# Kernel tuning notes

Measured on AMD Instinct MI355X. Metric: run time of the kernel, lower is better.

Reference implementation:

```python
import jax, jax.numpy as jnp
import numpy as np
import math

B, S, H = 2, 4096, 768
NH, HD = 12, 64  # num heads, head dim


def setup_inputs() -> dict:
    key = jax.random.key(0)
    ks = jax.random.split(key, 4)
    scale = 1.0 / math.sqrt(H)
    return {
        "hidden_states": jax.random.normal(ks[0], (B, S, H), jnp.float32),
        "attention_mask": jnp.zeros((B, 1, 1, S), jnp.float32),
        "Wq": jax.random.normal(ks[1], (H, H), jnp.float32) * scale,
        "bq": jnp.zeros((H,), jnp.float32),
        "Wk": jax.random.normal(ks[2], (H, H), jnp.float32) * scale,
        "bk": jnp.zeros((H,), jnp.float32),
        "Wv": jax.random.normal(ks[3], (H, H), jnp.float32) * scale,
        "bv": jnp.zeros((H,), jnp.float32),
    }


def reference(hidden_states, attention_mask, Wq, bq, Wk, bk, Wv, bv):
    # Linear projections (torch nn.Linear: x @ W.T + b)
    q = hidden_states @ Wq.T + bq  # [B,S,H]
    k = hidden_states @ Wk.T + bk
    v = hidden_states @ Wv.T + bv
    # split heads -> [B, NH, S, HD]
    def split(x):
        return x.reshape(B, S, NH, HD).transpose(0, 2, 1, 3)
    qh, kh, vh = split(q), split(k), split(v)
    scores = jnp.einsum('bhqd,bhkd->bhqk', qh, kh) / math.sqrt(HD)
    scores = scores + attention_mask  # additive mask, broadcast
    probs = jax.nn.softmax(scores, axis=-1)
    # dropout prob = 0.0 (inference) -> identity
    ctx = jnp.einsum('bhqk,bhkd->bhqd', probs, vh)
    ctx = ctx.transpose(0, 2, 1, 3).reshape(B, S, H)
    return ctx
```

## Files before the change

kernel.cpp:

```cpp
#include <hip/hip_runtime.h>
#include <hip/hip_bf16.h>

typedef float f32x4 __attribute__((ext_vector_type(4)));
typedef float f32x16 __attribute__((ext_vector_type(16)));
typedef short short8 __attribute__((ext_vector_type(8)));

#define LOG2E 1.44269504088896340736f

__device__ __forceinline__ ushort f2bf(float f){
  unsigned u = __builtin_bit_cast(unsigned, f);
  u = (u + 0x7fffu + ((u >> 16) & 1u)) >> 16;
  return (ushort)u;
}

__device__ __forceinline__ float exp2_hw(float x){
  float r; asm("v_exp_f32 %0, %1" : "=v"(r) : "v"(x)); return r;
}

__device__ __forceinline__ double pk_add(double a, double b){
  double d; asm("v_pk_add_f32 %0, %1, %2" : "=v"(d) : "v"(a), "v"(b)); return d;
}
__device__ __forceinline__ double pk_mul(double a, double b){
  double d; asm("v_pk_mul_f32 %0, %1, %2" : "=v"(d) : "v"(a), "v"(b)); return d;
}
__device__ __forceinline__ uint cvtpk_bf16(float lo, float hi){
  uint r; asm("v_cvt_pk_bf16_f32 %0, %1, %2" : "=v"(r) : "v"(lo), "v"(hi)); return r;
}
__device__ __forceinline__ double f2d(float x, float y){
  union { float f[2]; double d; } u; u.f[0] = x; u.f[1] = y; return u.d;
}
__device__ __forceinline__ float fmax3(float a, float b, float c){
  return fmaxf(fmaxf(a, b), c);
}

union F16u { f32x16 v; double d[8]; float f[16]; };

__global__ void prep_kernel(const float* __restrict__ hidden,
                            const float* __restrict__ Wq,
                            const float* __restrict__ Wk,
                            const float* __restrict__ Wv,
                            const float* __restrict__ mask,
                            ushort* __restrict__ Xb,
                            ushort* __restrict__ Wqb,
                            ushort* __restrict__ Wkb,
                            ushort* __restrict__ Wvb,
                            float* __restrict__ maskL){
  const int bid = blockIdx.x;
  if (bid < 6144 + 3*576){
    const float* src; ushort* dst; int i;
    if (bid < 6144){
      src = hidden; dst = Xb;  i = bid*256 + threadIdx.x;
    } else if (bid < 6144 + 576){
      src = Wq; dst = Wqb;     i = (bid - 6144)*256 + threadIdx.x;
    } else if (bid < 6144 + 1152){
      src = Wk; dst = Wkb;     i = (bid - 6720)*256 + threadIdx.x;
    } else {
      src = Wv; dst = Wvb;     i = (bid - 7296)*256 + threadIdx.x;
    }
    float4 v = ((const float4*)src)[i];
    ushort4 o; o.x = f2bf(v.x); o.y = f2bf(v.y); o.z = f2bf(v.z); o.w = f2bf(v.w);
    ((ushort4*)dst)[i] = o;
  } else {
    int i = (bid - 7872)*256 + threadIdx.x;
    float4 v = ((const float4*)mask)[i];
    float4 o;
    o.x = v.x * LOG2E; o.y = v.y * LOG2E; o.z = v.z * LOG2E; o.w = v.w * LOG2E;
    ((float4*)maskL)[i] = o;
  }
}

__global__ __launch_bounds__(256) void qkv_fused(const ushort* __restrict__ Xb,
                                                 const ushort* __restrict__ Wqb,
                                                 const ushort* __restrict__ Wkb,
                                                 const ushort* __restrict__ Wvb,
                                                 const float* __restrict__ bqp,
                                                 const float* __restrict__ bkp,
                                                 const float* __restrict__ bvp,
                                                 ushort* __restrict__ Qo,
                                                 ushort* __restrict__ Ko,
                                                 ushort* __restrict__ Vto,
                                                 float qscale){
  __shared__ ushort Xs[128*64];
  __shared__ ushort Ws[128*64];
  const int sel = blockIdx.y / 6;
  const int m0 = blockIdx.x * 128, n0 = (blockIdx.y % 6) * 128;
  const ushort* Wb  = (sel == 0) ? Wqb : (sel == 1) ? Wkb : Wvb;
  const float* bias = (sel == 0) ? bqp : (sel == 1) ? bkp : bvp;
  const int tid = threadIdx.x, w = tid >> 6, lane = tid & 63;
  const int r = lane & 15, g = lane >> 4;
  const int wr = (w >> 1) * 64, wc = (w & 1) * 64;
  const int lrow = lane >> 3;
  const int gk = (lane & 7) ^ lrow;
  f32x4 acc[4][4] = {};
  for (int k0 = 0; k0 < 768; k0 += 64){
    #pragma unroll
    for (int p = 0; p < 4; p++){
      int rowb = p*32 + w*8;
      int row = rowb + lrow;
      __builtin_amdgcn_global_load_lds(
        (const uint4*)(Xb + (size_t)(m0+row)*768 + k0 + gk*8),
        (uint4*)((char*)Xs + rowb*128), 16, 0, 0);
      __builtin_amdgcn_global_load_lds(
        (const uint4*)(Wb + (size_t)(n0+row)*768 + k0 + gk*8),
        (uint4*)((char*)Ws + rowb*128), 16, 0, 0);
    }
    __syncthreads();
    #pragma unroll
    for (int ks = 0; ks < 2; ks++){
      short8 af[4], bf[4];
      int bo = ks*64 + g*16;
      #pragma unroll
      for (int i = 0; i < 4; i++){
        int rowa = wr + i*16 + r;
        af[i] = *(const short8*)((char*)Xs + rowa*128 + (bo ^ ((rowa&7)<<4)));
        int rowb2 = wc + i*16 + r;
        bf[i] = *(const short8*)((char*)Ws + rowb2*128 + (bo ^ ((rowb2&7)<<4)));
      }
      #pragma unroll
      for (int i = 0; i < 4; i++)
        #pragma unroll
        for (int j = 0; j < 4; j++)
          acc[i][j] = __builtin_amdgcn_mfma_f32_16x16x32_bf16(af[i], bf[j], acc[i][j], 0,0,0);
    }
    __syncthreads();
  }
  if (sel < 2){
    ushort* Out = sel ? Ko : Qo;
    float scale = sel ? 1.0f : qscale;
    #pragma unroll
    for (int i = 0; i < 4; i++){
      #pragma unroll
      for (int j = 0; j < 4; j++){
        int col = n0 + wc + j*16 + r;
        float bv = bias[col];
        int rowb = m0 + wr + i*16 + g*4;
        #pragma unroll
        for (int q = 0; q < 4; q++)
          Out[(size_t)(rowb+q)*768 + col] = f2bf((acc[i][j][q] + bv) * scale);
      }
    }
  } else {
    #pragma unroll
    for (int i = 0; i < 4; i++){
      #pragma unroll
      for (int j = 0; j < 4; j++){
        int col = n0 + wc + j*16 + r;
        float bv = bias[col];
        int rowb = m0 + wr + i*16 + g*4;
        ushort4 o;
        o.x = f2bf(acc[i][j][0] + bv);
        o.y = f2bf(acc[i][j][1] + bv);
        o.z = f2bf(acc[i][j][2] + bv);
        o.w = f2bf(acc[i][j][3] + bv);
        size_t vrow = (size_t)((rowb >> 12) * 768 + col);
        *(ushort4*)(Vto + vrow * 4096 + (rowb & 4095)) = o;
      }
    }
  }
}

__global__ __launch_bounds__(256, 3) void flash_attn(const ushort* __restrict__ Qb,
                                                     const ushort* __restrict__ Kb,
                                                     const ushort* __restrict__ Vt,
                                                     const float* __restrict__ maskL,
                                                     ushort* __restrict__ part0,
                                                     ushort* __restrict__ part1,
                                                     float2* __restrict__ lm){
  __shared__ ushort SMEM[16384];
  const int tid = threadIdx.x, w = tid >> 6, lane = tid & 63;
  const int q = lane & 31, hi = lane >> 5;
  const int swq = (q & 7) << 4;
  const int h = blockIdx.y, b = blockIdx.z;
  const int qt = blockIdx.x >> 1, half = blockIdx.x & 1;
  const int q0 = qt * 128 + w * 32;
  char* sm = (char*)SMEM;

  short8 bq[4];
  {
    const ushort* qp = Qb + (size_t)(b*4096 + q0 + q)*768 + h*64 + hi*8;
    #pragma unroll
    for (int kd = 0; kd < 4; kd++) bq[kd] = *(const short8*)(qp + 16*kd);
  }
  const ushort* Kbase = Kb + (size_t)(b*4096 + half*2048)*768 + h*64;
  const ushort* Vbase = Vt + (size_t)(b*768 + h*64)*4096 + half*2048;

  const int row0 = tid >> 3, cir = tid & 7;
  const int row1 = row0 + 32;
  const int wb0 = row0*128 + ((cir*16) ^ ((row0&7)<<4));
  const int wb1 = row1*128 + ((cir*16) ^ ((row1&7)<<4));
  const ushort* kp0 = Kbase + (size_t)row0*768 + cir*8;
  const ushort* kp1 = Kbase + (size_t)row1*768 + cir*8;
  const ushort* vp0 = Vbase + (size_t)row0*4096 + cir*8;
  const ushort* vp1 = Vbase + (size_t)row1*4096 + cir*8;

  int off4[4];
  #pragma unroll
  for (int kd = 0; kd < 4; kd++)
    off4[kd] = q*128 + ((32*kd + 16*hi) ^ swq);

  uint4 k0r = *(const uint4*)kp0, k1r = *(const uint4*)kp1;
  uint4 v0r = *(const uint4*)vp0, v1r = *(const uint4*)vp1;
  *(uint4*)(sm + wb0) = k0r;           *(uint4*)(sm + wb1) = k1r;
  *(uint4*)(sm + 16384 + wb0) = v0r;   *(uint4*)(sm + 16384 + wb1) = v1r;
  k0r = *(const uint4*)(kp0 + (size_t)64*768);
  k1r = *(const uint4*)(kp1 + (size_t)64*768);
  v0r = *(const uint4*)(vp0 + 64);
  v1r = *(const uint4*)(vp1 + 64);
  __syncthreads();

  F16u c0, c1;
  { f32x16 zz = {}; c0.v = zz; c1.v = zz; }
  float mrun = -1e30f, lrun = 0.f;

  for (int t = 0; t < 32; t++){
    const int tb = (t & 1) << 13;
    const char* kb = sm + tb;
    const char* vb = kb + 16384;
    __builtin_amdgcn_s_setprio(1);
    f32x16 z0 = {}, z1 = {};
    #pragma unroll
    for (int kd = 0; kd < 4; kd++){
      short8 ak = *(const short8*)(kb + off4[kd]);
      z0 = __builtin_amdgcn_mfma_f32_32x32x16_bf16(ak, bq[kd], z0, 0,0,0);
    }
    #pragma unroll
    for (int kd = 0; kd < 4; kd++){
      short8 ak = *(const short8*)(kb + 4096 + off4[kd]);
      z1 = __builtin_amdgcn_mfma_f32_32x32x16_bf16(ak, bq[kd], z1, 0,0,0);
    }
    __builtin_amdgcn_s_setprio(0);
    F16u s0, s1; s0.v = z0; s1.v = z1;
    if (t < 31){
      char* wbuf = sm + (tb ^ 8192);
      *(uint4*)(wbuf + wb0) = k0r;           *(uint4*)(wbuf + wb1) = k1r;
      *(uint4*)(wbuf + 16384 + wb0) = v0r;   *(uint4*)(wbuf + 16384 + wb1) = v1r;
    }
    if (t < 30){
      const size_t kn = (size_t)(t+2) * 64;
      k0r = *(const uint4*)(kp0 + kn*768);
      k1r = *(const uint4*)(kp1 + kn*768);
      v0r = *(const uint4*)(vp0 + kn);
      v1r = *(const uint4*)(vp1 + kn);
    }
    const float* mrow = maskL + b*4096 + half*2048 + t*64 + hi*4;
    #pragma unroll
    for (int eq = 0; eq < 4; eq++){
      float4 m0v = *(const float4*)(mrow + eq*8);
      s0.d[2*eq]   = pk_add(s0.d[2*eq],   f2d(m0v.x, m0v.y));
      s0.d[2*eq+1] = pk_add(s0.d[2*eq+1], f2d(m0v.z, m0v.w));
      float4 m1v = *(const float4*)(mrow + 32 + eq*8);
      s1.d[2*eq]   = pk_add(s1.d[2*eq],   f2d(m1v.x, m1v.y));
      s1.d[2*eq+1] = pk_add(s1.d[2*eq+1], f2d(m1v.z, m1v.w));
    }
    float ma = fmax3(s0.f[0], s0.f[1], s0.f[2]);
    float mb = fmax3(s0.f[3], s0.f[4], s0.f[5]);
    ma = fmax3(ma, s0.f[6], s0.f[7]);
    mb = fmax3(mb, s0.f[8], s0.f[9]);
    ma = fmax3(ma, s0.f[10], s0.f[11]);
    mb = fmax3(mb, s0.f[12], s0.f[13]);
    ma = fmax3(ma, s0.f[14], s0.f[15]);
    mb = fmax3(mb, s1.f[0], s1.f[1]);
    ma = fmax3(ma, s1.f[2], s1.f[3]);
    mb = fmax3(mb, s1.f[4], s1.f[5]);
    ma = fmax3(ma, s1.f[6], s1.f[7]);
    mb = fmax3(mb, s1.f[8], s1.f[9]);
    ma = fmax3(ma, s1.f[10], s1.f[11]);
    mb = fmax3(mb, s1.f[12], s1.f[13]);
    float mt = fmax3(ma, s1.f[14], fmaxf(mb, s1.f[15]));
    mt = fmaxf(mt, __shfl_xor(mt, 32, 64));
    if (!__all(mt <= mrun + 11.5415603f)){
      float mnew = fmaxf(mrun, mt);
      float alpha = exp2_hw(mrun - mnew);
      mrun = mnew;
      lrun *= alpha;
      double al2 = f2d(alpha, alpha);
      #pragma unroll
      for (int i = 0; i < 8; i++){
        c0.d[i] = pk_mul(c0.d[i], al2);
        c1.d[i] = pk_mul(c1.d[i], al2);
      }
    }
    double msub = f2d(-mrun, -mrun);
    #pragma unroll
    for (int i = 0; i < 8; i++){
      s0.d[i] = pk_add(s0.d[i], msub);
      s1.d[i] = pk_add(s1.d[i], msub);
    }
    #pragma unroll
    for (int e = 0; e < 16; e++){
      s0.f[e] = exp2_hw(s0.f[e]);
      s1.f[e] = exp2_hw(s1.f[e]);
    }
    double t00 = pk_add(s0.d[0], s0.d[1]), t01 = pk_add(s0.d[2], s0.d[3]);
    double t02 = pk_add(s0.d[4], s0.d[5]), t03 = pk_add(s0.d[6], s0.d[7]);
    double t10 = pk_add(s1.d[0], s1.d[1]), t11 = pk_add(s1.d[2], s1.d[3]);
    double t12 = pk_add(s1.d[4], s1.d[5]), t13 = pk_add(s1.d[6], s1.d[7]);
    double u0 = pk_add(t00, t01), u1 = pk_add(t02, t03);
    double u2 = pk_add(t10, t11), u3 = pk_add(t12, t13);
    double wsum = pk_add(pk_add(u0, u1), pk_add(u2, u3));
    {
      union { double d; float f[2]; } uw; uw.d = wsum;
      float rs = uw.f[0] + uw.f[1];
      rs += __shfl_xor(rs, 32, 64);
      lrun += rs;
    }
    short8 bp[4];
    {
      uint pw[8];
      #pragma unroll
      for (int u = 0; u < 8; u++) pw[u] = cvtpk_bf16(s0.f[2*u], s0.f[2*u+1]);
      #pragma unroll
      for (int u2 = 0; u2 < 2; u2++){
        uint x0 = pw[4*u2+0], x1 = pw[4*u2+1], x2 = pw[4*u2+2], x3 = pw[4*u2+3];
        asm("v_permlane32_swap_b32 %0, %1" : "+v"(x0), "+v"(x2));
        asm("v_permlane32_swap_b32 %0, %1" : "+v"(x1), "+v"(x3));
        union { uint u[4]; short8 v; } bb;
        bb.u[0] = x0; bb.u[1] = x1; bb.u[2] = x2; bb.u[3] = x3;
        bp[u2] = bb.v;
      }
      #pragma unroll
      for (int u = 0; u < 8; u++) pw[u] = cvtpk_bf16(s1.f[2*u], s1.f[2*u+1]);
      #pragma unroll
      for (int u2 = 0; u2 < 2; u2++){
        uint x0 = pw[4*u2+0], x1 = pw[4*u2+1], x2 = pw[4*u2+2], x3 = pw[4*u2+3];
        asm("v_permlane32_swap_b32 %0, %1" : "+v"(x0), "+v"(x2));
        asm("v_permlane32_swap_b32 %0, %1" : "+v"(x1), "+v"(x3));
        union { uint u[4]; short8 v; } bb;
        bb.u[0] = x0; bb.u[1] = x1; bb.u[2] = x2; bb.u[3] = x3;
        bp[2+u2] = bb.v;
      }
    }
    __builtin_amdgcn_s_setprio(1);
    #pragma unroll
    for (int kk = 0; kk < 4; kk++){
      short8 av = *(const short8*)(vb + off4[kk]);
      c0.v = __builtin_amdgcn_mfma_f32_32x32x16_bf16(av, bp[kk], c0.v, 0,0,0);
    }
    #pragma unroll
    for (int kk = 0; kk < 4; kk++){
      short8 av = *(const short8*)(vb + 4096 + off4[kk]);
      c1.v = __builtin_amdgcn_mfma_f32_32x32x16_bf16(av, bp[kk], c1.v, 0,0,0);
    }
    __builtin_amdgcn_s_setprio(0);
    __syncthreads();
  }
  ushort* part = half ? part1 : part0;
  size_t orow = (size_t)(b*4096 + q0 + q) * 768 + h*64;
  #pragma unroll
  for (int eq = 0; eq < 4; eq++){
    uint2 o;
    o.x = cvtpk_bf16(c0.f[4*eq+0], c0.f[4*eq+1]);
    o.y = cvtpk_bf16(c0.f[4*eq+2], c0.f[4*eq+3]);
    *(uint2*)(part + orow + eq*8 + hi*4) = o;
  }
  #pragma unroll
  for (int eq = 0; eq < 4; eq++){
    uint2 o;
    o.x = cvtpk_bf16(c1.f[4*eq+0], c1.f[4*eq+1]);
    o.y = cvtpk_bf16(c1.f[4*eq+2], c1.f[4*eq+3]);
    *(uint2*)(part + orow + 32 + eq*8 + hi*4) = o;
  }
  if (hi == 0){
    int idx = ((half*2 + b)*12 + h)*4096 + (q0 + q);
    lm[idx] = make_float2(mrun, lrun);
  }
}

__global__ void merge_kernel(const ushort* __restrict__ p0, const ushort* __restrict__ p1,
                             const float2* __restrict__ lm, float* __restrict__ out){
  int i = blockIdx.x * 256 + threadIdx.x;
  const int nf4 = 2*4096*768/4;
  if (i >= nf4) return;
  int f = i * 4;
  int b = f / (4096*768);
  int rem = f - b*(4096*768);
  int qrow = rem / 768;
  int col = rem - qrow*768;
  int head = col >> 6;
  float2 L0 = lm[((    b)*12 + head)*4096 + qrow];
  float2 L1 = lm[((2 + b)*12 + head)*4096 + qrow];
  float M = fmaxf(L0.x, L1.x);
  float e0 = exp2f(L0.x - M), e1 = exp2f(L1.x - M);
  float inv = 1.0f / (L0.y*e0 + L1.y*e1);
  float s0 = e0 * inv, s1 = e1 * inv;
  uint2 a = ((const uint2*)p0)[i];
  uint2 c = ((const uint2*)p1)[i];
  float4 o;
  o.x = __builtin_bit_cast(float, a.x << 16)         * s0 + __builtin_bit_cast(float, c.x << 16)         * s1;
  o.y = __builtin_bit_cast(float, a.x & 0xffff0000u) * s0 + __builtin_bit_cast(float, c.x & 0xffff0000u) * s1;
  o.z = __builtin_bit_cast(float, a.y << 16)         * s0 + __builtin_bit_cast(float, c.y << 16)         * s1;
  o.w = __builtin_bit_cast(float, a.y & 0xffff0000u) * s0 + __builtin_bit_cast(float, c.y & 0xffff0000u) * s1;
  ((float4*)out)[i] = o;
}

extern "C" void kernel_launch(void* const* d_in, const int* in_sizes, int n_in,
                              void* d_out, int out_size, void* d_ws, size_t ws_size,
                              hipStream_t stream){
  const float* hidden = (const float*)d_in[0];
  const float* mask   = (const float*)d_in[1];
  const float* Wq     = (const float*)d_in[2];
  const float* bq     = (const float*)d_in[3];
  const float* Wk     = (const float*)d_in[4];
  const float* bk     = (const float*)d_in[5];
  const float* Wv     = (const float*)d_in[6];
  const float* bv     = (const float*)d_in[7];
  char* ws = (char*)d_ws;
  ushort* Xb    = (ushort*)(ws);
  ushort* Wqb   = (ushort*)(ws + 12582912);
  ushort* Wkb   = (ushort*)(ws + 13762560);
  ushort* Wvb   = (ushort*)(ws + 14942208);
  ushort* Qb    = (ushort*)(ws + 16121856);
  ushort* Kb    = (ushort*)(ws + 28704768);
  ushort* Vtb   = (ushort*)(ws + 41287680);
  float*  maskL = (float*)(ws + 53870592);
  ushort* part0 = (ushort*)(ws + 53903360);
  ushort* part1 = (ushort*)(ws + 66486272);
  float2* lmbuf = (float2*)(ws + 79069184);

  prep_kernel<<<7880, 256, 0, stream>>>(hidden, Wq, Wk, Wv, mask,
                                        Xb, Wqb, Wkb, Wvb, maskL);

  dim3 gg(64, 18);
  qkv_fused<<<gg, 256, 0, stream>>>(Xb, Wqb, Wkb, Wvb, bq, bk, bv,
                                    Qb, Kb, Vtb, 0.125f * LOG2E);

  dim3 ga(64, 12, 2);
  flash_attn<<<ga, 256, 0, stream>>>(Qb, Kb, Vtb, maskL, part0, part1, lmbuf);
  merge_kernel<<<6144, 256, 0, stream>>>(part0, part1, lmbuf, (float*)d_out);
}
```

Before: 219.4 us.

## Load K/V tiles directly into LDS with global_load_lds double buffering

Replaces the register-staged K/V prefetch (global load to VGPRs, then ds_write) with direct global-to-LDS async loads. The per-lane source addresses are pre-swizzled so the contiguous per-wave LDS layout matches the XOR-swizzled read pattern. Loads for the next tile are issued at the start of each iteration into the other buffer. This frees VGPRs and removes the LDS write instructions, at the risk of different wait/sync behaviour, since the existing barrier must now cover the async LDS writes.

```diff
diff --git a/kernel.cpp b/kernel.cpp
--- a/kernel.cpp
+++ b/kernel.cpp
@@ -184,28 +184,24 @@
   const ushort* Kbase = Kb + (size_t)(b*4096 + half*2048)*768 + h*64;
   const ushort* Vbase = Vt + (size_t)(b*768 + h*64)*4096 + half*2048;
 
-  const int row0 = tid >> 3, cir = tid & 7;
-  const int row1 = row0 + 32;
-  const int wb0 = row0*128 + ((cir*16) ^ ((row0&7)<<4));
-  const int wb1 = row1*128 + ((cir*16) ^ ((row1&7)<<4));
-  const ushort* kp0 = Kbase + (size_t)row0*768 + cir*8;
-  const ushort* kp1 = Kbase + (size_t)row1*768 + cir*8;
-  const ushort* vp0 = Vbase + (size_t)row0*4096 + cir*8;
-  const ushort* vp1 = Vbase + (size_t)row1*4096 + cir*8;
+  const int lr = lane >> 3;
+  const int gk = (lane & 7) ^ lr;
+  const ushort* kg0 = Kbase + (size_t)(w*8 + lr)*768 + gk*8;
+  const ushort* kg1 = kg0 + (size_t)32*768;
+  const ushort* vg0 = Vbase + (size_t)(w*8 + lr)*4096 + gk*8;
+  const ushort* vg1 = vg0 + (size_t)32*4096;
+  const int wofs = w*1024;
 
   int off4[4];
   #pragma unroll
   for (int kd = 0; kd < 4; kd++)
     off4[kd] = q*128 + ((32*kd + 16*hi) ^ swq);
 
-  uint4 k0r = *(const uint4*)kp0, k1r = *(const uint4*)kp1;
-  uint4 v0r = *(const uint4*)vp0, v1r = *(const uint4*)vp1;
-  *(uint4*)(sm + wb0) = k0r;           *(uint4*)(sm + wb1) = k1r;
-  *(uint4*)(sm + 16384 + wb0) = v0r;   *(uint4*)(sm + 16384 + wb1) = v1r;
-  k0r = *(const uint4*)(kp0 + (size_t)64*768);
-  k1r = *(const uint4*)(kp1 + (size_t)64*768);
-  v0r = *(const uint4*)(vp0 + 64);
-  v1r = *(const uint4*)(vp1 + 64);
+  __builtin_amdgcn_global_load_lds((const uint4*)kg0, (uint4*)(sm + wofs),                16, 0, 0);
+  __builtin_amdgcn_global_load_lds((const uint4*)kg1, (uint4*)(sm + wofs + 4096),         16, 0, 0);
+  __builtin_amdgcn_global_load_lds((const uint4*)vg0, (uint4*)(sm + wofs + 16384),        16, 0, 0);
+  __builtin_amdgcn_global_load_lds((const uint4*)vg1, (uint4*)(sm + wofs + 16384 + 4096), 16, 0, 0);
+  kg0 += 49152; kg1 += 49152; vg0 += 64; vg1 += 64;
   __syncthreads();
 
   F16u c0, c1;
@@ -216,6 +212,14 @@
     const int tb = (t & 1) << 13;
     const char* kb = sm + tb;
     const char* vb = kb + 16384;
+    if (t < 31){
+      char* nb = sm + (tb ^ 8192) + wofs;
+      __builtin_amdgcn_global_load_lds((const uint4*)kg0, (uint4*)nb,                  16, 0, 0);
+      __builtin_amdgcn_global_load_lds((const uint4*)kg1, (uint4*)(nb + 4096),         16, 0, 0);
+      __builtin_amdgcn_global_load_lds((const uint4*)vg0, (uint4*)(nb + 16384),        16, 0, 0);
+      __builtin_amdgcn_global_load_lds((const uint4*)vg1, (uint4*)(nb + 16384 + 4096), 16, 0, 0);
+      kg0 += 49152; kg1 += 49152; vg0 += 64; vg1 += 64;
+    }
     __builtin_amdgcn_s_setprio(1);
     f32x16 z0 = {}, z1 = {};
     #pragma unroll
@@ -230,18 +234,6 @@
     }
     __builtin_amdgcn_s_setprio(0);
     F16u s0, s1; s0.v = z0; s1.v = z1;
-    if (t < 31){
-      char* wbuf = sm + (tb ^ 8192);
-      *(uint4*)(wbuf + wb0) = k0r;           *(uint4*)(wbuf + wb1) = k1r;
-      *(uint4*)(wbuf + 16384 + wb0) = v0r;   *(uint4*)(wbuf + 16384 + wb1) = v1r;
-    }
-    if (t < 30){
-      const size_t kn = (size_t)(t+2) * 64;
-      k0r = *(const uint4*)(kp0 + kn*768);
-      k1r = *(const uint4*)(kp1 + kn*768);
-      v0r = *(const uint4*)(vp0 + kn);
-      v1r = *(const uint4*)(vp1 + kn);
-    }
     const float* mrow = maskL + b*4096 + half*2048 + t*64 + hi*4;
     #pragma unroll
     for (int eq = 0; eq < 4; eq++){
```

New measurement: 225.3 us. 2.7% more time.
